# Performance work log

Measured on AMD Instinct MI355X. Metric: run time of the kernel, lower is better.

Reference implementation:

```python
import jax, jax.numpy as jnp
import numpy as np

B, L, V = 2048, 200, 100000
EMB_DIM = 32      # emb_session_dim / emb_loc_dim (hardcoded 32 in __init__)
TIME_DIM = 128    # config['model']['timeemb']
LOC_DIM = 32
COND = TIME_DIM + LOC_DIM  # 160
NUM_STEPS = 50
MASK_TIME = 48    # pe[pos == 48] = 0 in the 2-D branch


def _time_embedding(pos, d_model):
    # sinusoidal embedding, interleaved sin/cos exactly as the torch code
    div = 1.0 / jnp.power(10000.0, jnp.arange(0, d_model, 2, dtype=jnp.float32) / d_model)
    ang = pos[..., None].astype(jnp.float32) * div           # [..., d_model//2]
    pe = jnp.zeros(pos.shape + (d_model,), jnp.float32)
    pe = pe.at[..., 0::2].set(jnp.sin(ang)).at[..., 1::2].set(jnp.cos(ang))
    return pe


def setup_inputs() -> dict:
    key = jax.random.key(0)
    ks = jax.random.split(key, 12)
    tp = jax.random.randint(ks[0], (B,), 0, 48, dtype=jnp.int32)
    loc = jax.random.randint(ks[1], (B,), 1, V + 1)            # 1-based loc ids
    emb = jax.random.normal(ks[2], (B, EMB_DIM), jnp.float32)
    s = jax.random.randint(ks[3], (B, L), 1, V + 1)
    tt = jax.random.randint(ks[4], (B, L), 0, 49)              # 48 == padding slot
    ST_traj = jnp.stack([s, tt], axis=-1)                      # [B, L, 2]
    loc_emb_all = jax.random.normal(ks[5], (V, LOC_DIM), jnp.float32) * 0.1
    noise = jax.random.normal(ks[6], (B, EMB_DIM), jnp.float32)
    t = jax.random.randint(ks[7], (B,), 0, NUM_STEPS)
    sc = COND ** -0.5
    w1 = jax.random.normal(ks[8], (COND, COND), jnp.float32) * sc
    w2 = jax.random.normal(ks[9], (COND, COND), jnp.float32) * sc
    b2 = jnp.zeros((COND,), jnp.float32)
    wc = jax.random.normal(ks[10], (COND,), jnp.float32) * sc
    beta = np.linspace(0.0001 ** 0.5, 0.5 ** 0.5, NUM_STEPS) ** 2  # 'quad' schedule
    alpha_hat = jnp.asarray(np.cumprod(1.0 - beta), jnp.float32)
    return {"tp": tp, "loc": loc, "emb": emb, "ST_traj": ST_traj,
            "loc_emb_all": loc_emb_all, "noise": noise, "t": t,
            "w1": w1, "w2": w2, "b2": b2, "wc": wc, "alpha_hat": alpha_hat}


def reference(tp, loc, emb, ST_traj, loc_emb_all, noise, t, w1, w2, b2, wc, alpha_hat):
    # --- diffusion noising (calc_loss prelude) ---
    a = alpha_hat[t][:, None]                                   # [B, 1]
    noisy = jnp.sqrt(a) * emb + jnp.sqrt(1.0 - a) * noise       # [B, EMB_DIM]

    # --- get_ST_info: sinusoid + single fused gather (replaces per-element index_select loop) ---
    te = _time_embedding(tp, TIME_DIM)                          # [B, TIME_DIM] (1-D branch: no mask)
    le = loc_emb_all[loc - 1]                                   # [B, LOC_DIM]
    side = jnp.concatenate([te, le], axis=-1)                   # [B, COND]
    ST_info = jnp.broadcast_to(side[:, :, None], (B, COND, EMB_DIM))

    # --- get_user_info: trajectory embed + soft_attn ---
    s = ST_traj[..., 0]
    ts = ST_traj[..., 1]
    te2 = _time_embedding(ts, TIME_DIM)                         # [B, L, TIME_DIM]
    te2 = jnp.where((ts == MASK_TIME)[..., None], 0.0, te2)     # pe[pos == 48] = 0
    le2 = loc_emb_all[s - 1]                                    # [B, L, LOC_DIM] fused gather
    ue = jnp.concatenate([le2, te2], axis=-1)                   # [B, L, COND]
    mean_e = jnp.mean(ue, axis=1, keepdims=True)                # [B, 1, COND]
    attn = jax.nn.sigmoid(mean_e @ w1.T + ue @ w2.T + b2)       # [B, L, COND]
    score = attn @ wc                                           # [B, L]  (weight_c)
    uemb = jnp.einsum('bl,bld->bd', score, ue)                  # [B, COND]
    user_info = jnp.broadcast_to(uemb[:, :, None], (B, COND, EMB_DIM))

    # pack: [B, 2*COND + 1, EMB_DIM]
    return jnp.concatenate([ST_info, user_info, noisy[:, None, :]], axis=1)
```

## Files before the change

kernel.cpp:

```cpp
#include <hip/hip_runtime.h>
#include <hip/hip_bf16.h>

#define LSEQ   200
#define LPAD   208
#define EMB    32
#define TDIM   128
#define COND   160
#define ROWS   321
#define MASK_T 48

typedef __attribute__((ext_vector_type(8))) short  short8;
typedef __attribute__((ext_vector_type(4))) float  f32x4;

#define WAIT_LGKM() asm volatile("s_waitcnt lgkmcnt(0)" ::: "memory")

__device__ __forceinline__ float bf2f(unsigned short u) {
    union { unsigned int i; float f; } v; v.i = ((unsigned int)u) << 16; return v.f;
}
__device__ __forceinline__ unsigned int f2bf(float f) {
    union { float f; unsigned int i; } v; v.f = f;
    unsigned int x = v.i;
    return ((x + 0x7fffu + ((x >> 16) & 1u)) >> 16);
}
__device__ __forceinline__ unsigned int pack2(float lo, float hi) {
    return f2bf(lo) | (f2bf(hi) << 16);
}
__device__ __forceinline__ short8 pack8(f32x4 a, f32x4 b) {
    union { short8 s; unsigned int u[4]; } r;
    r.u[0] = pack2(a[0], a[1]); r.u[1] = pack2(a[2], a[3]);
    r.u[2] = pack2(b[0], b[1]); r.u[3] = pack2(b[2], b[3]);
    return r.s;
}

template<int CTRL>
__device__ __forceinline__ float dpp_add(float v) {
    const int x = __builtin_amdgcn_update_dpp(0, __float_as_int(v), CTRL, 0xf, 0xf, true);
    return v + __int_as_float(x);
}
__device__ __forceinline__ float red16(float v) {
    v = dpp_add<0x128>(v);
    v = dpp_add<0x124>(v);
    v = dpp_add<0x122>(v);
    v = dpp_add<0x121>(v);
    return v;
}

__global__ void prep(const float* __restrict__ w1, const float* __restrict__ w2,
                     unsigned short* __restrict__ te_tab, float* __restrict__ T1t,
                     unsigned short* __restrict__ te_t, unsigned short* __restrict__ T2w) {
    __shared__ float te128[TDIM];
    const int t = blockIdx.x, tid = threadIdx.x;
    if (tid < 64) {
        const float dv = __expf(-0.14391156f * (float)tid);
        const float a  = (float)t * dv;
        const float s  = __sinf(a), c = __cosf(a);
        te128[2 * tid] = s; te128[2 * tid + 1] = c;
        ((unsigned int*)te_tab)[t * 64 + tid] = pack2(s, c);
    }
    __syncthreads();
    if (tid < COND) {
        float s1 = 0.0f, s2 = 0.0f;
        const float* w1r = w1 + tid * COND + EMB;
        const float* w2r = w2 + tid * COND + EMB;
        #pragma unroll 8
        for (int j = 0; j < TDIM; ++j) {
            s1 = fmaf(te128[j], w1r[j], s1);
            s2 = fmaf(te128[j], w2r[j], s2);
        }
        if (t == MASK_T) { s1 = 0.0f; s2 = 0.0f; }
        T1t[tid * 52 + t] = s1;
        T2w[t * 192 + (tid & 15) * 12 + (tid >> 4)] = (unsigned short)f2bf(s2);
    }
    if (tid < TDIM) te_t[tid * 52 + t] = (unsigned short)f2bf(te128[tid]);
}

__global__ __launch_bounds__(256)
void fused_wave(const int*   __restrict__ tp,
                const int*   __restrict__ loc,
                const float* __restrict__ emb,
                const int*   __restrict__ st,
                const float* __restrict__ loc_emb,
                const float* __restrict__ noise,
                const int*   __restrict__ tstep,
                const float* __restrict__ w1,
                const float* __restrict__ w2,
                const unsigned short* __restrict__ te_tab,
                const float* __restrict__ T1t,
                const unsigned short* __restrict__ te_t,
                const unsigned short* __restrict__ T2w,
                const float* __restrict__ b2,
                const float* __restrict__ wc,
                const float* __restrict__ alpha_hat,
                float* __restrict__ out, int nb)
{
    __shared__ unsigned short ttr[4][LPAD];
    __shared__ int            ssr[4][LPAD];
    __shared__ float          scoreA[4][LPAD];
    __shared__ float          su[4][320];
    __shared__ float          mloc[4][32];
    __shared__ float          m1A[4][COND];
    __shared__ float          cntA[4][52];
    __shared__ float          sbA[4][52];

    const int tid  = threadIdx.x;
    const int w    = tid >> 6, lane = tid & 63;
    const int b    = blockIdx.x * 4 + w;
    if (b >= nb) return;
    const int lc = lane & 15, lg = lane >> 4;

    unsigned short* ttrW = ttr[w];
    int*   ssrW = ssr[w];
    float* scoreW = scoreA[w];
    float* suW  = su[w];
    float* mlocW = mloc[w];
    float* m1W  = m1A[w];
    float* cntW = cntA[w];
    float* sbW  = sbA[w];
    float* outb = out + (size_t)b * (ROWS * EMB);

    if (lane < 52) { cntW[lane] = 0.0f; sbW[lane] = 0.0f; }
    if (lane < 32) {
        const ushort4 tv = *(const ushort4*)(te_tab + tp[b] * TDIM + lane * 4);
        f32x4 s4 = { bf2f(tv.x), bf2f(tv.y), bf2f(tv.z), bf2f(tv.w) };
        *(f32x4*)(suW + lane * 4) = s4;
    } else if (lane < 40) {
        const f32x4 lv = *(const f32x4*)(loc_emb + (size_t)(loc[b] - 1) * EMB + (lane - 32) * 4);
        *(f32x4*)(suW + 128 + (lane - 32) * 4) = lv;
    } else if (lane < 48) {
        const int e4 = lane - 40;
        const float a = alpha_hat[tstep[b]];
        const float sa = sqrtf(a), sn = sqrtf(1.0f - a);
        const f32x4 ev = *(const f32x4*)(emb + (size_t)b * EMB + e4 * 4);
        const f32x4 nv = *(const f32x4*)(noise + (size_t)b * EMB + e4 * 4);
        f32x4 r = { sa*ev[0]+sn*nv[0], sa*ev[1]+sn*nv[1], sa*ev[2]+sn*nv[2], sa*ev[3]+sn*nv[3] };
        *(f32x4*)(outb + 320 * EMB + e4 * 4) = r;
    }

    int sA[4], tA[4];
    f32x4 mean8[8];
    #pragma unroll
    for (int j = 0; j < 8; ++j) mean8[j] = f32x4{0.f, 0.f, 0.f, 0.f};
    #pragma unroll
    for (int k = 0; k < 4; ++k) {
        const int r = lane + k * 64;
        sA[k] = 1; tA[k] = MASK_T;
        if (r < LSEQ) {
            const int2 sv = ((const int2*)st)[(size_t)b * LSEQ + r];
            sA[k] = sv.x; tA[k] = sv.y;
            ttrW[r] = (unsigned short)sv.y;
            ssrW[r] = sv.x;
            if (sv.y != MASK_T) atomicAdd(&cntW[sv.y], 1.0f);
            const f32x4* lr = (const f32x4*)(loc_emb + (size_t)(sv.x - 1) * EMB);
            #pragma unroll
            for (int j = 0; j < 8; ++j) mean8[j] += lr[j];
        } else if (r < LPAD) {
            ttrW[r] = 0; ssrW[r] = 1;
        }
    }
    #pragma unroll
    for (int s2 = 1; s2 < 64; s2 <<= 1) {
        #pragma unroll
        for (int j = 0; j < 8; ++j) {
            mean8[j][0] += __shfl_xor(mean8[j][0], s2);
            mean8[j][1] += __shfl_xor(mean8[j][1], s2);
            mean8[j][2] += __shfl_xor(mean8[j][2], s2);
            mean8[j][3] += __shfl_xor(mean8[j][3], s2);
        }
    }
    {
        f32x4* ml4 = (f32x4*)mlocW;
        if (lane == 0) ml4[0] = mean8[0];
        if (lane == 1) ml4[1] = mean8[1];
        if (lane == 2) ml4[2] = mean8[2];
        if (lane == 3) ml4[3] = mean8[3];
        if (lane == 4) ml4[4] = mean8[4];
        if (lane == 5) ml4[5] = mean8[5];
        if (lane == 6) ml4[6] = mean8[6];
        if (lane == 7) ml4[7] = mean8[7];
    }
    WAIT_LGKM();

    {
        f32x4 mm[8], cc[13];
        #pragma unroll
        for (int j = 0; j < 8; ++j)  mm[j] = ((const f32x4*)mlocW)[j];
        #pragma unroll
        for (int j = 0; j < 13; ++j) cc[j] = ((const f32x4*)cntW)[j];
        #pragma unroll
        for (int k = 0; k < 3; ++k) {
            const int c = lane + k * 64;
            if (c < COND) {
                f32x4 d = {0.f, 0.f, 0.f, 0.f};
                const f32x4* w1r = (const f32x4*)(w1 + (size_t)c * COND);
                #pragma unroll
                for (int j = 0; j < 8; ++j)  d += mm[j] * w1r[j];
                const f32x4* t1r = (const f32x4*)(T1t + c * 52);
                #pragma unroll
                for (int j = 0; j < 13; ++j) d += cc[j] * t1r[j];
                m1W[c] = b2[c] + (d[0] + d[1] + d[2] + d[3]) * 0.005f;
            }
        }
    }
    WAIT_LGKM();

    short8 bf[10]; float m1v[10], wcv[10];
    #pragma unroll
    for (int T = 0; T < 10; ++T) {
        const f32x4* r = (const f32x4*)(w2 + (size_t)(T * 16 + lc) * COND + lg * 8);
        bf[T]  = pack8(r[0], r[1]);
        m1v[T] = m1W[T * 16 + lc];
        wcv[T] = wc[T * 16 + lc];
    }

    int ssv[13];
    #pragma unroll
    for (int m = 0; m < 13; ++m) ssv[m] = ssrW[m * 16 + lc];

    #pragma unroll
    for (int m = 0; m < 13; ++m) {
        const ushort4 tq = *(const ushort4*)(ttrW + m * 16 + lg * 4);
        ushort4 t2q[4][3];
        #pragma unroll
        for (int r = 0; r < 4; ++r) {
            const int t = (r == 0) ? tq.x : (r == 1) ? tq.y : (r == 2) ? tq.z : tq.w;
            const unsigned short* t2r = T2w + t * 192 + lc * 12;
            t2q[r][0] = *(const ushort4*)(t2r);
            t2q[r][1] = *(const ushort4*)(t2r + 4);
            t2q[r][2] = *(const ushort4*)(t2r + 8);
        }
        const f32x4* ar = (const f32x4*)(loc_emb + (size_t)(ssv[m] - 1) * EMB + lg * 8);
        const short8 av = pack8(ar[0], ar[1]);

        f32x4 srow = {0.f, 0.f, 0.f, 0.f};
        #pragma unroll
        for (int T = 0; T < 10; ++T) {
            f32x4 acc = {0.f, 0.f, 0.f, 0.f};
            acc = __builtin_amdgcn_mfma_f32_16x16x32_bf16(av, bf[T], acc, 0, 0, 0);
            #pragma unroll
            for (int r = 0; r < 4; ++r) {
                const ushort4 q = t2q[r][T >> 2];
                const unsigned short t2u =
                    ((T & 3) == 0) ? q.x : ((T & 3) == 1) ? q.y : ((T & 3) == 2) ? q.z : q.w;
                const float x = acc[r] + m1v[T] + bf2f(t2u);
                srow[r] = fmaf(wcv[T], __builtin_amdgcn_rcpf(1.0f + __expf(-x)), srow[r]);
            }
        }
        srow[0] = red16(srow[0]); srow[1] = red16(srow[1]);
        srow[2] = red16(srow[2]); srow[3] = red16(srow[3]);
        if (lc == 0) *(f32x4*)(scoreW + m * 16 + lg * 4) = srow;
    }
    WAIT_LGKM();

    f32x4 u8[8];
    #pragma unroll
    for (int j = 0; j < 8; ++j) u8[j] = f32x4{0.f, 0.f, 0.f, 0.f};
    #pragma unroll
    for (int k = 0; k < 4; ++k) {
        const int r = lane + k * 64;
        if (r < LSEQ) {
            const float sc = scoreW[r];
            if (tA[k] != MASK_T) atomicAdd(&sbW[tA[k]], sc);
            const f32x4* lr = (const f32x4*)(loc_emb + (size_t)(sA[k] - 1) * EMB);
            #pragma unroll
            for (int j = 0; j < 8; ++j) u8[j] += sc * lr[j];
        }
    }
    #pragma unroll
    for (int s2 = 1; s2 < 64; s2 <<= 1) {
        #pragma unroll
        for (int j = 0; j < 8; ++j) {
            u8[j][0] += __shfl_xor(u8[j][0], s2);
            u8[j][1] += __shfl_xor(u8[j][1], s2);
            u8[j][2] += __shfl_xor(u8[j][2], s2);
            u8[j][3] += __shfl_xor(u8[j][3], s2);
        }
    }
    {
        f32x4* ul4 = (f32x4*)(suW + 160);
        if (lane == 0) ul4[0] = u8[0];
        if (lane == 1) ul4[1] = u8[1];
        if (lane == 2) ul4[2] = u8[2];
        if (lane == 3) ul4[3] = u8[3];
        if (lane == 4) ul4[4] = u8[4];
        if (lane == 5) ul4[5] = u8[5];
        if (lane == 6) ul4[6] = u8[6];
        if (lane == 7) ul4[7] = u8[7];
    }
    WAIT_LGKM();

    {
        f32x4 sbr[13];
        #pragma unroll
        for (int j = 0; j < 13; ++j) sbr[j] = ((const f32x4*)sbW)[j];
        #pragma unroll
        for (int k = 0; k < 2; ++k) {
            const int j = lane + k * 64;
            const unsigned short* ter = te_t + j * 52;
            float s = 0.0f;
            #pragma unroll
            for (int q = 0; q < 13; ++q) {
                const ushort4 tv = *(const ushort4*)(ter + q * 4);
                s = fmaf(sbr[q][0], bf2f(tv.x), s);
                s = fmaf(sbr[q][1], bf2f(tv.y), s);
                s = fmaf(sbr[q][2], bf2f(tv.z), s);
                s = fmaf(sbr[q][3], bf2f(tv.w), s);
            }
            suW[192 + j] = s;
        }
    }
    WAIT_LGKM();

    #pragma unroll 4
    for (int k = 0; k < 40; ++k) {
        const int idx = lane + k * 64;
        const int row = idx >> 3;
        const float v = suW[row];
        f32x4 vv = {v, v, v, v};
        *(f32x4*)(outb + row * EMB + (idx & 7) * 4) = vv;
    }
}

extern "C" void kernel_launch(void* const* d_in, const int* in_sizes, int n_in,
                              void* d_out, int out_size, void* d_ws, size_t ws_size,
                              hipStream_t stream) {
    const int*   tp        = (const int*)  d_in[0];
    const int*   loc       = (const int*)  d_in[1];
    const float* emb       = (const float*)d_in[2];
    const int*   st        = (const int*)  d_in[3];
    const float* loc_emb   = (const float*)d_in[4];
    const float* noise     = (const float*)d_in[5];
    const int*   tstep     = (const int*)  d_in[6];
    const float* w1        = (const float*)d_in[7];
    const float* w2        = (const float*)d_in[8];
    const float* b2        = (const float*)d_in[9];
    const float* wc        = (const float*)d_in[10];
    const float* alpha_hat = (const float*)d_in[11];
    float* out = (float*)d_out;

    char* ws = (char*)d_ws;
    float*          T1t    = (float*)ws;
    unsigned short* te_tab = (unsigned short*)(ws + 33280);
    unsigned short* te_t   = (unsigned short*)(ws + 45824);
    unsigned short* T2w    = (unsigned short*)(ws + 59136);

    prep<<<49, 256, 0, stream>>>(w1, w2, te_tab, T1t, te_t, T2w);

    const int nb = in_sizes[0];
    fused_wave<<<(nb + 3) / 4, 256, 0, stream>>>(tp, loc, emb, st, loc_emb, noise,
                                                 tstep, w1, w2, te_tab, T1t, te_t,
                                                 T2w, b2, wc, alpha_hat, out, nb);
}
```

Before: 75.83 us.

## Split each batch row across two waves and stage gathered embeddings in LDS as bf16

The work for one batch row moves from a single 64-lane wave to a 128-thread block of two waves. The waves split the sequence rows for the gathers and split the 160 output columns for the MFMA attention step, then combine partial scores with LDS atomics. Gathered loc_emb rows are packed to bf16 once in shared memory and reused for the MFMA operand and the weighted sum, which avoids re-gathering from global memory. The cost is block-level __syncthreads barriers, atomics on scores, bf16 rounding in the user-embedding sum, and a relaid T2 table.

```diff
diff --git a/kernel.cpp b/kernel.cpp
--- a/kernel.cpp
+++ b/kernel.cpp
@@ -8,14 +8,16 @@
 #define COND   160
 #define ROWS   321
 #define MASK_T 48
+#define LL_LDB 80
 
 typedef __attribute__((ext_vector_type(8))) short  short8;
 typedef __attribute__((ext_vector_type(4))) float  f32x4;
 
-#define WAIT_LGKM() asm volatile("s_waitcnt lgkmcnt(0)" ::: "memory")
-
 __device__ __forceinline__ float bf2f(unsigned short u) {
     union { unsigned int i; float f; } v; v.i = ((unsigned int)u) << 16; return v.f;
+}
+__device__ __forceinline__ float asf(unsigned int u) {
+    union { unsigned int i; float f; } v; v.i = u; return v.f;
 }
 __device__ __forceinline__ unsigned int f2bf(float f) {
     union { float f; unsigned int i; } v; v.f = f;
@@ -47,7 +49,7 @@
 
 __global__ void prep(const float* __restrict__ w1, const float* __restrict__ w2,
                      unsigned short* __restrict__ te_tab, float* __restrict__ T1t,
-                     unsigned short* __restrict__ te_t, unsigned short* __restrict__ T2w) {
+                     unsigned short* __restrict__ te_t, unsigned short* __restrict__ T2w2) {
     __shared__ float te128[TDIM];
     const int t = blockIdx.x, tid = threadIdx.x;
     if (tid < 64) {
@@ -69,252 +71,251 @@
         }
         if (t == MASK_T) { s1 = 0.0f; s2 = 0.0f; }
         T1t[tid * 52 + t] = s1;
-        T2w[t * 192 + (tid & 15) * 12 + (tid >> 4)] = (unsigned short)f2bf(s2);
+        const int tile = tid >> 4, lcc = tid & 15;
+        const int wg = (tile >= 5) ? 1 : 0, Tp = tile - 5 * wg;
+        T2w2[t * 256 + wg * 128 + lcc * 8 + Tp] = (unsigned short)f2bf(s2);
     }
     if (tid < TDIM) te_t[tid * 52 + t] = (unsigned short)f2bf(te128[tid]);
 }
 
-__global__ __launch_bounds__(256)
-void fused_wave(const int*   __restrict__ tp,
-                const int*   __restrict__ loc,
-                const float* __restrict__ emb,
-                const int*   __restrict__ st,
-                const float* __restrict__ loc_emb,
-                const float* __restrict__ noise,
-                const int*   __restrict__ tstep,
-                const float* __restrict__ w1,
-                const float* __restrict__ w2,
-                const unsigned short* __restrict__ te_tab,
-                const float* __restrict__ T1t,
-                const unsigned short* __restrict__ te_t,
-                const unsigned short* __restrict__ T2w,
-                const float* __restrict__ b2,
-                const float* __restrict__ wc,
-                const float* __restrict__ alpha_hat,
-                float* __restrict__ out, int nb)
+__global__ __launch_bounds__(128, 4)
+void fused2(const int*   __restrict__ tp,
+            const int*   __restrict__ loc,
+            const float* __restrict__ emb,
+            const int*   __restrict__ st,
+            const float* __restrict__ loc_emb,
+            const float* __restrict__ noise,
+            const int*   __restrict__ tstep,
+            const float* __restrict__ w1,
+            const float* __restrict__ w2,
+            const unsigned short* __restrict__ te_tab,
+            const float* __restrict__ T1t,
+            const unsigned short* __restrict__ te_t,
+            const unsigned short* __restrict__ T2w2,
+            const float* __restrict__ b2,
+            const float* __restrict__ wc,
+            const float* __restrict__ alpha_hat,
+            float* __restrict__ out)
 {
-    __shared__ unsigned short ttr[4][LPAD];
-    __shared__ int            ssr[4][LPAD];
-    __shared__ float          scoreA[4][LPAD];
-    __shared__ float          su[4][320];
-    __shared__ float          mloc[4][32];
-    __shared__ float          m1A[4][COND];
-    __shared__ float          cntA[4][52];
-    __shared__ float          sbA[4][52];
+    __shared__ __attribute__((aligned(16))) unsigned char LL[LPAD * LL_LDB];
+    __shared__ float scoreW[LSEQ];
+    __shared__ float su[320];
+    __shared__ float m1W[COND];
+    __shared__ float mupart[2][EMB];
+    __shared__ float cntsb[52];
+    __shared__ __attribute__((aligned(8))) unsigned short ttr[LPAD];
 
     const int tid  = threadIdx.x;
     const int w    = tid >> 6, lane = tid & 63;
-    const int b    = blockIdx.x * 4 + w;
-    if (b >= nb) return;
-    const int lc = lane & 15, lg = lane >> 4;
-
-    unsigned short* ttrW = ttr[w];
-    int*   ssrW = ssr[w];
-    float* scoreW = scoreA[w];
-    float* suW  = su[w];
-    float* mlocW = mloc[w];
-    float* m1W  = m1A[w];
-    float* cntW = cntA[w];
-    float* sbW  = sbA[w];
+    const int b    = blockIdx.x;
+    const int lc   = lane & 15, lg = lane >> 4;
+    const int rsub = lane >> 3, csub = lane & 7;
+    const int2* st2 = (const int2*)st;
     float* outb = out + (size_t)b * (ROWS * EMB);
 
-    if (lane < 52) { cntW[lane] = 0.0f; sbW[lane] = 0.0f; }
-    if (lane < 32) {
-        const ushort4 tv = *(const ushort4*)(te_tab + tp[b] * TDIM + lane * 4);
-        f32x4 s4 = { bf2f(tv.x), bf2f(tv.y), bf2f(tv.z), bf2f(tv.w) };
-        *(f32x4*)(suW + lane * 4) = s4;
-    } else if (lane < 40) {
-        const f32x4 lv = *(const f32x4*)(loc_emb + (size_t)(loc[b] - 1) * EMB + (lane - 32) * 4);
-        *(f32x4*)(suW + 128 + (lane - 32) * 4) = lv;
-    } else if (lane < 48) {
-        const int e4 = lane - 40;
-        const float a = alpha_hat[tstep[b]];
-        const float sa = sqrtf(a), sn = sqrtf(1.0f - a);
-        const f32x4 ev = *(const f32x4*)(emb + (size_t)b * EMB + e4 * 4);
-        const f32x4 nv = *(const f32x4*)(noise + (size_t)b * EMB + e4 * 4);
-        f32x4 r = { sa*ev[0]+sn*nv[0], sa*ev[1]+sn*nv[1], sa*ev[2]+sn*nv[2], sa*ev[3]+sn*nv[3] };
-        *(f32x4*)(outb + 320 * EMB + e4 * 4) = r;
-    }
-
-    int sA[4], tA[4];
-    f32x4 mean8[8];
-    #pragma unroll
-    for (int j = 0; j < 8; ++j) mean8[j] = f32x4{0.f, 0.f, 0.f, 0.f};
-    #pragma unroll
-    for (int k = 0; k < 4; ++k) {
-        const int r = lane + k * 64;
-        sA[k] = 1; tA[k] = MASK_T;
-        if (r < LSEQ) {
-            const int2 sv = ((const int2*)st)[(size_t)b * LSEQ + r];
-            sA[k] = sv.x; tA[k] = sv.y;
-            ttrW[r] = (unsigned short)sv.y;
-            ssrW[r] = sv.x;
-            if (sv.y != MASK_T) atomicAdd(&cntW[sv.y], 1.0f);
-            const f32x4* lr = (const f32x4*)(loc_emb + (size_t)(sv.x - 1) * EMB);
-            #pragma unroll
-            for (int j = 0; j < 8; ++j) mean8[j] += lr[j];
-        } else if (r < LPAD) {
-            ttrW[r] = 0; ssrW[r] = 1;
-        }
-    }
-    #pragma unroll
-    for (int s2 = 1; s2 < 64; s2 <<= 1) {
-        #pragma unroll
-        for (int j = 0; j < 8; ++j) {
-            mean8[j][0] += __shfl_xor(mean8[j][0], s2);
-            mean8[j][1] += __shfl_xor(mean8[j][1], s2);
-            mean8[j][2] += __shfl_xor(mean8[j][2], s2);
-            mean8[j][3] += __shfl_xor(mean8[j][3], s2);
-        }
-    }
+    if (w == 0) {
+        if (lane < 32) {
+            const ushort4 tv = *(const ushort4*)(te_tab + tp[b] * TDIM + lane * 4);
+            f32x4 s4 = { bf2f(tv.x), bf2f(tv.y), bf2f(tv.z), bf2f(tv.w) };
+            *(f32x4*)(su + lane * 4) = s4;
+        } else if (lane < 40) {
+            *(f32x4*)(su + 128 + (lane - 32) * 4) =
+                *(const f32x4*)(loc_emb + (size_t)(loc[b] - 1) * EMB + (lane - 32) * 4);
+        } else if (lane < 48) {
+            const int e4 = lane - 40;
+            const float a  = alpha_hat[tstep[b]];
+            const float sa = sqrtf(a), sn = sqrtf(1.0f - a);
+            const f32x4 ev = *(const f32x4*)(emb + (size_t)b * EMB + e4 * 4);
+            const f32x4 nv = *(const f32x4*)(noise + (size_t)b * EMB + e4 * 4);
+            f32x4 r = { sa*ev[0]+sn*nv[0], sa*ev[1]+sn*nv[1],
+                        sa*ev[2]+sn*nv[2], sa*ev[3]+sn*nv[3] };
+            *(f32x4*)(outb + 320 * EMB + e4 * 4) = r;
+        }
+    } else {
+        if (lane < 52) cntsb[lane] = 0.0f;
+        if (lane < 50) {
+            f32x4 z = {0.f, 0.f, 0.f, 0.f};
+            *(f32x4*)(scoreW + lane * 4) = z;
+        }
+        if (lane >= 52 && lane < 60) {
+            const int r = 200 + lane - 52;
+            uint4 z = make_uint4(0, 0, 0, 0);
+            *(uint4*)(LL + r * LL_LDB)      = z;
+            *(uint4*)(LL + r * LL_LDB + 16) = z;
+            *(uint4*)(LL + r * LL_LDB + 32) = z;
+            *(uint4*)(LL + r * LL_LDB + 48) = z;
+            ttr[r] = 0;
+        }
+    }
+    __syncthreads();
+
+    int tA0, tA1 = MASK_T;
     {
-        f32x4* ml4 = (f32x4*)mlocW;
-        if (lane == 0) ml4[0] = mean8[0];
-        if (lane == 1) ml4[1] = mean8[1];
-        if (lane == 2) ml4[2] = mean8[2];
-        if (lane == 3) ml4[3] = mean8[3];
-        if (lane == 4) ml4[4] = mean8[4];
-        if (lane == 5) ml4[5] = mean8[5];
-        if (lane == 6) ml4[6] = mean8[6];
-        if (lane == 7) ml4[7] = mean8[7];
-    }
-    WAIT_LGKM();
+        const int r = w * 100 + lane;
+        const int2 sv = st2[(size_t)b * LSEQ + r];
+        ttr[r] = (unsigned short)sv.y;
+        tA0 = sv.y;
+        if (sv.y != MASK_T) atomicAdd(&cntsb[sv.y], 1.0f);
+        if (lane < 36) {
+            const int r2 = r + 64;
+            const int2 sv2 = st2[(size_t)b * LSEQ + r2];
+            ttr[r2] = (unsigned short)sv2.y;
+            tA1 = sv2.y;
+            if (sv2.y != MASK_T) atomicAdd(&cntsb[sv2.y], 1.0f);
+        }
+    }
+
+    f32x4 macc = {0.f, 0.f, 0.f, 0.f};
+    #pragma unroll
+    for (int i = 0; i < 13; ++i) {
+        const int rr = i * 8 + rsub;
+        if (rr < 100) {
+            const int row = w * 100 + rr;
+            const int s0 = st2[(size_t)b * LSEQ + row].x - 1;
+            const f32x4 v = *(const f32x4*)(loc_emb + (size_t)s0 * EMB + csub * 4);
+            macc += v;
+            uint2 pv = make_uint2(pack2(v[0], v[1]), pack2(v[2], v[3]));
+            *(uint2*)(LL + row * LL_LDB + csub * 8) = pv;
+        }
+    }
+    #pragma unroll
+    for (int sh = 8; sh < 64; sh <<= 1) {
+        macc[0] += __shfl_xor(macc[0], sh);
+        macc[1] += __shfl_xor(macc[1], sh);
+        macc[2] += __shfl_xor(macc[2], sh);
+        macc[3] += __shfl_xor(macc[3], sh);
+    }
+    if (rsub == 0) *(f32x4*)(&mupart[w][csub * 4]) = macc;
+    __syncthreads();
 
     {
-        f32x4 mm[8], cc[13];
-        #pragma unroll
-        for (int j = 0; j < 8; ++j)  mm[j] = ((const f32x4*)mlocW)[j];
-        #pragma unroll
-        for (int j = 0; j < 13; ++j) cc[j] = ((const f32x4*)cntW)[j];
-        #pragma unroll
-        for (int k = 0; k < 3; ++k) {
-            const int c = lane + k * 64;
+        f32x4 mm[8];
+        #pragma unroll
+        for (int j = 0; j < 8; ++j)
+            mm[j] = ((const f32x4*)mupart[0])[j] + ((const f32x4*)mupart[1])[j];
+        #pragma unroll
+        for (int k = 0; k < 2; ++k) {
+            const int c = tid + k * 128;
             if (c < COND) {
                 f32x4 d = {0.f, 0.f, 0.f, 0.f};
                 const f32x4* w1r = (const f32x4*)(w1 + (size_t)c * COND);
                 #pragma unroll
-                for (int j = 0; j < 8; ++j)  d += mm[j] * w1r[j];
+                for (int j = 0; j < 8; ++j) d += mm[j] * w1r[j];
                 const f32x4* t1r = (const f32x4*)(T1t + c * 52);
                 #pragma unroll
-                for (int j = 0; j < 13; ++j) d += cc[j] * t1r[j];
+                for (int q = 0; q < 13; ++q)
+                    d += ((const f32x4*)cntsb)[q] * t1r[q];
                 m1W[c] = b2[c] + (d[0] + d[1] + d[2] + d[3]) * 0.005f;
             }
         }
     }
-    WAIT_LGKM();
-
-    short8 bf[10]; float m1v[10], wcv[10];
-    #pragma unroll
-    for (int T = 0; T < 10; ++T) {
-        const f32x4* r = (const f32x4*)(w2 + (size_t)(T * 16 + lc) * COND + lg * 8);
+    __syncthreads();
+
+    if (w == 1 && lane < 52) cntsb[lane] = 0.0f;
+
+    short8 bf[5]; float m1v[5], wcv[5];
+    #pragma unroll
+    for (int T = 0; T < 5; ++T) {
+        const int c = (5 * w + T) * 16 + lc;
+        const f32x4* r = (const f32x4*)(w2 + (size_t)c * COND + lg * 8);
         bf[T]  = pack8(r[0], r[1]);
-        m1v[T] = m1W[T * 16 + lc];
-        wcv[T] = wc[T * 16 + lc];
-    }
-
-    int ssv[13];
-    #pragma unroll
-    for (int m = 0; m < 13; ++m) ssv[m] = ssrW[m * 16 + lc];
-
-    #pragma unroll
+        m1v[T] = m1W[c];
+        wcv[T] = wc[c];
+    }
+
     for (int m = 0; m < 13; ++m) {
-        const ushort4 tq = *(const ushort4*)(ttrW + m * 16 + lg * 4);
-        ushort4 t2q[4][3];
+        const short8 av = *(const short8*)(LL + (m * 16 + lc) * LL_LDB + lg * 16);
+        const ushort4 tq = *(const ushort4*)(ttr + m * 16 + lg * 4);
+        ushort4 q0[4], q1[4];
         #pragma unroll
         for (int r = 0; r < 4; ++r) {
             const int t = (r == 0) ? tq.x : (r == 1) ? tq.y : (r == 2) ? tq.z : tq.w;
-            const unsigned short* t2r = T2w + t * 192 + lc * 12;
-            t2q[r][0] = *(const ushort4*)(t2r);
-            t2q[r][1] = *(const ushort4*)(t2r + 4);
-            t2q[r][2] = *(const ushort4*)(t2r + 8);
-        }
-        const f32x4* ar = (const f32x4*)(loc_emb + (size_t)(ssv[m] - 1) * EMB + lg * 8);
-        const short8 av = pack8(ar[0], ar[1]);
-
+            const unsigned short* p = T2w2 + t * 256 + w * 128 + lc * 8;
+            q0[r] = *(const ushort4*)(p);
+            q1[r] = *(const ushort4*)(p + 4);
+        }
         f32x4 srow = {0.f, 0.f, 0.f, 0.f};
         #pragma unroll
-        for (int T = 0; T < 10; ++T) {
+        for (int T = 0; T < 5; ++T) {
             f32x4 acc = {0.f, 0.f, 0.f, 0.f};
             acc = __builtin_amdgcn_mfma_f32_16x16x32_bf16(av, bf[T], acc, 0, 0, 0);
             #pragma unroll
             for (int r = 0; r < 4; ++r) {
-                const ushort4 q = t2q[r][T >> 2];
                 const unsigned short t2u =
-                    ((T & 3) == 0) ? q.x : ((T & 3) == 1) ? q.y : ((T & 3) == 2) ? q.z : q.w;
+                    (T == 0) ? q0[r].x : (T == 1) ? q0[r].y :
+                    (T == 2) ? q0[r].z : (T == 3) ? q0[r].w : q1[r].x;
                 const float x = acc[r] + m1v[T] + bf2f(t2u);
                 srow[r] = fmaf(wcv[T], __builtin_amdgcn_rcpf(1.0f + __expf(-x)), srow[r]);
             }
         }
         srow[0] = red16(srow[0]); srow[1] = red16(srow[1]);
         srow[2] = red16(srow[2]); srow[3] = red16(srow[3]);
-        if (lc == 0) *(f32x4*)(scoreW + m * 16 + lg * 4) = srow;
-    }
-    WAIT_LGKM();
-
-    f32x4 u8[8];
-    #pragma unroll
-    for (int j = 0; j < 8; ++j) u8[j] = f32x4{0.f, 0.f, 0.f, 0.f};
-    #pragma unroll
-    for (int k = 0; k < 4; ++k) {
-        const int r = lane + k * 64;
-        if (r < LSEQ) {
-            const float sc = scoreW[r];
-            if (tA[k] != MASK_T) atomicAdd(&sbW[tA[k]], sc);
-            const f32x4* lr = (const f32x4*)(loc_emb + (size_t)(sA[k] - 1) * EMB);
+        if (lc == 0) {
             #pragma unroll
-            for (int j = 0; j < 8; ++j) u8[j] += sc * lr[j];
-        }
-    }
-    #pragma unroll
-    for (int s2 = 1; s2 < 64; s2 <<= 1) {
-        #pragma unroll
-        for (int j = 0; j < 8; ++j) {
-            u8[j][0] += __shfl_xor(u8[j][0], s2);
-            u8[j][1] += __shfl_xor(u8[j][1], s2);
-            u8[j][2] += __shfl_xor(u8[j][2], s2);
-            u8[j][3] += __shfl_xor(u8[j][3], s2);
-        }
-    }
+            for (int r = 0; r < 4; ++r) {
+                const int row = m * 16 + lg * 4 + r;
+                if (row < LSEQ) atomicAdd(&scoreW[row], srow[r]);
+            }
+        }
+    }
+    __syncthreads();
+
     {
-        f32x4* ul4 = (f32x4*)(suW + 160);
-        if (lane == 0) ul4[0] = u8[0];
-        if (lane == 1) ul4[1] = u8[1];
-        if (lane == 2) ul4[2] = u8[2];
-        if (lane == 3) ul4[3] = u8[3];
-        if (lane == 4) ul4[4] = u8[4];
-        if (lane == 5) ul4[5] = u8[5];
-        if (lane == 6) ul4[6] = u8[6];
-        if (lane == 7) ul4[7] = u8[7];
-    }
-    WAIT_LGKM();
+        const int r = w * 100 + lane;
+        const float sc = scoreW[r];
+        if (tA0 != MASK_T) atomicAdd(&cntsb[tA0], sc);
+        if (lane < 36) {
+            const float sc2 = scoreW[r + 64];
+            if (tA1 != MASK_T) atomicAdd(&cntsb[tA1], sc2);
+        }
+    }
+    f32x4 uacc = {0.f, 0.f, 0.f, 0.f};
+    #pragma unroll
+    for (int i = 0; i < 13; ++i) {
+        const int rr = i * 8 + rsub;
+        if (rr < 100) {
+            const int row = w * 100 + rr;
+            const float sc = scoreW[row];
+            const uint2 pv = *(const uint2*)(LL + row * LL_LDB + csub * 8);
+            uacc[0] = fmaf(sc, asf(pv.x << 16), uacc[0]);
+            uacc[1] = fmaf(sc, asf(pv.x & 0xffff0000u), uacc[1]);
+            uacc[2] = fmaf(sc, asf(pv.y << 16), uacc[2]);
+            uacc[3] = fmaf(sc, asf(pv.y & 0xffff0000u), uacc[3]);
+        }
+    }
+    #pragma unroll
+    for (int sh = 8; sh < 64; sh <<= 1) {
+        uacc[0] += __shfl_xor(uacc[0], sh);
+        uacc[1] += __shfl_xor(uacc[1], sh);
+        uacc[2] += __shfl_xor(uacc[2], sh);
+        uacc[3] += __shfl_xor(uacc[3], sh);
+    }
+    if (rsub == 0) *(f32x4*)(&mupart[w][csub * 4]) = uacc;
+    __syncthreads();
 
     {
-        f32x4 sbr[13];
-        #pragma unroll
-        for (int j = 0; j < 13; ++j) sbr[j] = ((const f32x4*)sbW)[j];
-        #pragma unroll
-        for (int k = 0; k < 2; ++k) {
-            const int j = lane + k * 64;
-            const unsigned short* ter = te_t + j * 52;
-            float s = 0.0f;
-            #pragma unroll
-            for (int q = 0; q < 13; ++q) {
-                const ushort4 tv = *(const ushort4*)(ter + q * 4);
-                s = fmaf(sbr[q][0], bf2f(tv.x), s);
-                s = fmaf(sbr[q][1], bf2f(tv.y), s);
-                s = fmaf(sbr[q][2], bf2f(tv.z), s);
-                s = fmaf(sbr[q][3], bf2f(tv.w), s);
-            }
-            suW[192 + j] = s;
-        }
-    }
-    WAIT_LGKM();
-
-    #pragma unroll 4
-    for (int k = 0; k < 40; ++k) {
-        const int idx = lane + k * 64;
+        const int j = tid;
+        const unsigned short* ter = te_t + j * 52;
+        float s = 0.0f;
+        #pragma unroll
+        for (int q = 0; q < 13; ++q) {
+            const f32x4 sq = ((const f32x4*)cntsb)[q];
+            const ushort4 tv = *(const ushort4*)(ter + q * 4);
+            s = fmaf(sq[0], bf2f(tv.x), s);
+            s = fmaf(sq[1], bf2f(tv.y), s);
+            s = fmaf(sq[2], bf2f(tv.z), s);
+            s = fmaf(sq[3], bf2f(tv.w), s);
+        }
+        su[192 + j] = s;
+    }
+    if (tid < 32) su[160 + tid] = mupart[0][tid] + mupart[1][tid];
+    __syncthreads();
+
+    #pragma unroll
+    for (int k = 0; k < 20; ++k) {
+        const int idx = tid + k * 128;
         const int row = idx >> 3;
-        const float v = suW[row];
+        const float v = su[row];
         f32x4 vv = {v, v, v, v};
         *(f32x4*)(outb + row * EMB + (idx & 7) * 4) = vv;
     }
@@ -341,12 +342,12 @@
     float*          T1t    = (float*)ws;
     unsigned short* te_tab = (unsigned short*)(ws + 33280);
     unsigned short* te_t   = (unsigned short*)(ws + 45824);
-    unsigned short* T2w    = (unsigned short*)(ws + 59136);
-
-    prep<<<49, 256, 0, stream>>>(w1, w2, te_tab, T1t, te_t, T2w);
+    unsigned short* T2w2   = (unsigned short*)(ws + 59136);
+
+    prep<<<49, 256, 0, stream>>>(w1, w2, te_tab, T1t, te_t, T2w2);
 
     const int nb = in_sizes[0];
-    fused_wave<<<(nb + 3) / 4, 256, 0, stream>>>(tp, loc, emb, st, loc_emb, noise,
-                                                 tstep, w1, w2, te_tab, T1t, te_t,
-                                                 T2w, b2, wc, alpha_hat, out, nb);
-}
+    fused2<<<nb, 128, 0, stream>>>(tp, loc, emb, st, loc_emb, noise, tstep,
+                                   w1, w2, te_tab, T1t, te_t, T2w2,
+                                   b2, wc, alpha_hat, out);
+}
```

New measurement: 65.64 us. 13.4% less time.
